# Performance work log

Measured on AMD Instinct MI355X. Metric: run time of the kernel, lower is better.

The kernel has to match this reference:

```python
import jax, jax.numpy as jnp
import numpy as np

N_EMBD = 1024
N_HEAD = 16
HEAD_DIM = N_EMBD // N_HEAD
NEG = -1e9


def setup_inputs() -> dict:
    key = jax.random.key(0)
    ks = jax.random.split(key, 5)
    B, S = 2, 2048
    x = jax.random.normal(ks[0], (B, S, N_EMBD), dtype=jnp.float32)
    # qkv_proj: Linear(n_embd, 3*n_embd) -> weight used as x @ W_qkv (W stored [in, out])
    scale = 1.0 / np.sqrt(N_EMBD)
    W_qkv = jax.random.normal(ks[1], (N_EMBD, 3 * N_EMBD), dtype=jnp.float32) * scale
    b_qkv = jax.random.normal(ks[2], (3 * N_EMBD,), dtype=jnp.float32) * 0.02
    W_out = jax.random.normal(ks[3], (N_EMBD, N_EMBD), dtype=jnp.float32) * scale
    b_out = jax.random.normal(ks[4], (N_EMBD,), dtype=jnp.float32) * 0.02
    return {"x": x, "W_qkv": W_qkv, "b_qkv": b_qkv, "W_out": W_out, "b_out": b_out}


def reference(x, W_qkv, b_qkv, W_out, b_out):
    B, S, E = x.shape
    qkv = x @ W_qkv + b_qkv                      # [B,S,3E]
    q, k, v = jnp.split(qkv, 3, axis=-1)
    # [B,S,E] -> [B,H,S,D]
    def split_heads(t):
        return t.reshape(B, S, N_HEAD, HEAD_DIM).transpose(0, 2, 1, 3)
    q, k, v = split_heads(q), split_heads(k), split_heads(v)
    scores = jnp.einsum("bhqd,bhkd->bhqk", q, k) / jnp.sqrt(jnp.float32(HEAD_DIM))
    causal = jnp.tril(jnp.ones((S, S), dtype=bool))
    scores = jnp.where(causal, scores, NEG)
    attn = jax.nn.softmax(scores, axis=-1)
    out = jnp.einsum("bhqk,bhkd->bhqd", attn, v)  # [B,H,S,D]
    out = out.transpose(0, 2, 1, 3).reshape(B, S, E)
    return out @ W_out + b_out
```

## Files before the change

kernel.cpp:

```cpp
#include <hip/hip_runtime.h>
#include <hip/hip_bf16.h>

#define BATCH 2
#define SEQ   2048
#define EMBD  1024
#define NHEAD 16
#define HDIM  64
#define QKV3  (3 * EMBD)

typedef __attribute__((ext_vector_type(8))) __bf16 bf16x8;
typedef __attribute__((ext_vector_type(4))) __bf16 bf16x4;
typedef __attribute__((ext_vector_type(4))) float f32x4;

#define QSCALE 0.18033688011112043f

__global__ __launch_bounds__(256) void cast_f32_bf16(
    const float* __restrict__ in, __bf16* __restrict__ out)
{
    int i = (blockIdx.x * 256 + threadIdx.x) * 8;
    float4 a = *(const float4*)&in[i];
    float4 b = *(const float4*)&in[i + 4];
    bf16x8 o;
    o[0] = (__bf16)a.x; o[1] = (__bf16)a.y; o[2] = (__bf16)a.z; o[3] = (__bf16)a.w;
    o[4] = (__bf16)b.x; o[5] = (__bf16)b.y; o[6] = (__bf16)b.z; o[7] = (__bf16)b.w;
    *(bf16x8*)&out[i] = o;
}

__global__ __launch_bounds__(256) void transpose_cast_bf16(
    const float* __restrict__ in, __bf16* __restrict__ out, int K, int N)
{
    __shared__ float t[64][65];
    const int k0 = blockIdx.y * 64, n0 = blockIdx.x * 64;
    const int tid = threadIdx.x;
    #pragma unroll
    for (int p = 0; p < 4; p++) {
        int kr = p * 16 + (tid >> 4);
        int c4 = (tid & 15) * 4;
        float4 v = *(const float4*)&in[(size_t)(k0 + kr) * N + n0 + c4];
        t[kr][c4] = v.x; t[kr][c4 + 1] = v.y; t[kr][c4 + 2] = v.z; t[kr][c4 + 3] = v.w;
    }
    __syncthreads();
    #pragma unroll
    for (int p = 0; p < 4; p++) {
        int nr = p * 16 + (tid >> 4);
        int k4 = (tid & 15) * 4;
        bf16x4 o;
        o[0] = (__bf16)t[k4 + 0][nr];
        o[1] = (__bf16)t[k4 + 1][nr];
        o[2] = (__bf16)t[k4 + 2][nr];
        o[3] = (__bf16)t[k4 + 3][nr];
        *(bf16x4*)&out[(size_t)(n0 + nr) * K + k0 + k4] = o;
    }
}

__global__ __launch_bounds__(256) void transpose_v_bf16(
    const __bf16* __restrict__ qkv, __bf16* __restrict__ vt)
{
    __shared__ __bf16 t[64][72];
    const int k0 = blockIdx.x * 64;
    const int bh = blockIdx.y;
    const int b = bh >> 4, h = bh & 15;
    const size_t base = (size_t)b * SEQ * QKV3 + 2 * EMBD + h * HDIM;
    const int tid = threadIdx.x;
    #pragma unroll
    for (int it = 0; it < 2; it++) {
        int flat = it * 256 + tid;
        int kr = flat >> 3;
        int d0 = (flat & 7) * 8;
        bf16x8 v = *(const bf16x8*)&qkv[base + (size_t)(k0 + kr) * QKV3 + d0];
        #pragma unroll
        for (int i = 0; i < 8; i++) t[kr][d0 + i] = v[i];
    }
    __syncthreads();
    #pragma unroll
    for (int it = 0; it < 2; it++) {
        int flat = it * 256 + tid;
        int d  = flat >> 3;
        int kc = (flat & 7) * 8;
        bf16x8 o;
        #pragma unroll
        for (int i = 0; i < 8; i++) o[i] = t[kc + i][d];
        *(bf16x8*)&vt[((size_t)bh * 64 + d) * SEQ + k0 + kc] = o;
    }
}

template<bool OUT_BF16>
__global__ __launch_bounds__(256) void gemm_bt_mfma(
    const __bf16* __restrict__ A,
    const __bf16* __restrict__ Bt,
    const float* __restrict__ bias,
    void* __restrict__ Cv,
    int M, int N, int K, int nscale)
{
    __shared__ __align__(16) __bf16 As[128 * 32];
    __shared__ __align__(16) __bf16 Bs[128 * 32];

    const int tid  = threadIdx.x;
    const int lane = tid & 63;
    const int wave = tid >> 6;
    const int wm = (wave >> 1) * 64;
    const int wn = (wave & 1) * 64;
    const int m0 = blockIdx.y * 128;
    const int n0 = blockIdx.x * 128;
    const int lm = lane & 15;
    const int kq = lane >> 4;

    f32x4 acc[4][4] = {};

    for (int k0 = 0; k0 < K; k0 += 32) {
        __syncthreads();
        #pragma unroll
        for (int r = 0; r < 2; r++) {
            int flat = r * 256 + tid;
            int row  = flat >> 2;
            int off  = (flat & 3) * 16;
            const char* ga = (const char*)(A + (size_t)(m0 + row) * K + k0) + off;
            char* la = (char*)As + flat * 16;
            __builtin_amdgcn_global_load_lds(
                (const __attribute__((address_space(1))) void*)ga,
                (__attribute__((address_space(3))) void*)la, 16, 0, 0);
            const char* gb = (const char*)(Bt + (size_t)(n0 + row) * K + k0) + off;
            char* lb = (char*)Bs + flat * 16;
            __builtin_amdgcn_global_load_lds(
                (const __attribute__((address_space(1))) void*)gb,
                (__attribute__((address_space(3))) void*)lb, 16, 0, 0);
        }
        __syncthreads();

        bf16x8 af[4], bf[4];
        #pragma unroll
        for (int t = 0; t < 4; t++) {
            af[t] = *(const bf16x8*)&As[(wm + t * 16 + lm) * 32 + kq * 8];
            bf[t] = *(const bf16x8*)&Bs[(wn + t * 16 + lm) * 32 + kq * 8];
        }
        #pragma unroll
        for (int i = 0; i < 4; i++)
            #pragma unroll
            for (int j = 0; j < 4; j++)
                acc[i][j] = __builtin_amdgcn_mfma_f32_16x16x32_bf16(
                    af[i], bf[j], acc[i][j], 0, 0, 0);
    }

    const int r0 = kq * 4;
    #pragma unroll
    for (int i = 0; i < 4; i++) {
        #pragma unroll
        for (int j = 0; j < 4; j++) {
            int col = n0 + wn + j * 16 + lm;
            float bv = bias[col];
            float sc = (col < nscale) ? QSCALE : 1.0f;
            #pragma unroll
            for (int r = 0; r < 4; r++) {
                int row = m0 + wm + i * 16 + r0 + r;
                float val = (acc[i][j][r] + bv) * sc;
                if (OUT_BF16) ((__bf16*)Cv)[(size_t)row * N + col] = (__bf16)val;
                else          ((float*)Cv)[(size_t)row * N + col] = val;
            }
        }
    }
}

__global__ __launch_bounds__(256, 3) void attn_kpar_mfma(
    const __bf16* __restrict__ qkv, const __bf16* __restrict__ vt,
    __bf16* __restrict__ attn)
{
    __shared__ __align__(16) char smem[16896];

    const int tid  = threadIdx.x;
    const int wave = tid >> 6;
    const int lane = tid & 63;
    const int quad = lane >> 4;
    const int c    = lane & 15;

    const int bh = blockIdx.x;
    const int b  = bh >> 4;
    const int h  = bh & 15;
    const int qblk = (int)(gridDim.y - 1) - blockIdx.y;
    const int q0 = qblk * 32;

    const size_t base = (size_t)b * SEQ * QKV3;
    const int hoff = h * HDIM;
    const __bf16* vbase = vt + (size_t)bh * 64 * SEQ;

    bf16x8 aq[2][2];
    #pragma unroll
    for (int qf = 0; qf < 2; qf++) {
        const __bf16* qrow = qkv + base +
            (size_t)(q0 + qf * 16 + c) * QKV3 + hoff + quad * 8;
        aq[qf][0] = *(const bf16x8*)(qrow);
        aq[qf][1] = *(const bf16x8*)(qrow + 32);
    }

    f32x4 acc[2][4] = {};
    float lpart[2][4] = {};

    char* pbw = smem + wave * 4096;
    const int ntiles = q0 / 64 + 1;

    for (int t = wave; t < ntiles; t += 4) {
        const int k0 = t * 64;
        const bool diag = (t == ntiles - 1);

        bf16x8 bk[4][2];
        #pragma unroll
        for (int jj = 0; jj < 4; jj++) {
            const __bf16* krow = qkv + base +
                (size_t)(k0 + jj * 16 + c) * QKV3 + EMBD + hoff + quad * 8;
            bk[jj][0] = *(const bf16x8*)(krow);
            bk[jj][1] = *(const bf16x8*)(krow + 32);
        }
        bf16x8 bv[4][2];
        #pragma unroll
        for (int dd = 0; dd < 4; dd++) {
            const __bf16* vr = vbase + (size_t)(dd * 16 + c) * SEQ + k0 + quad * 8;
            bv[dd][0] = *(const bf16x8*)(vr);
            bv[dd][1] = *(const bf16x8*)(vr + 32);
        }

        #pragma unroll
        for (int jj = 0; jj < 4; jj++) {
            const int col = jj * 16 + c;
            const int kabs_c = k0 + col;
            const int ab = (col >> 5) * 1024 + ((col >> 3) & 3) * 256 + (col & 7) * 2;
            #pragma unroll
            for (int qf = 0; qf < 2; qf++) {
                f32x4 s = {};
                s = __builtin_amdgcn_mfma_f32_16x16x32_bf16(aq[qf][0], bk[jj][0], s, 0, 0, 0);
                s = __builtin_amdgcn_mfma_f32_16x16x32_bf16(aq[qf][1], bk[jj][1], s, 0, 0, 0);
                char* pq = pbw + qf * 2048 + ab;
                const int qabs0 = q0 + qf * 16 + quad * 4;
                #pragma unroll
                for (int r = 0; r < 4; r++) {
                    float p;
                    if (diag && (kabs_c > qabs0 + r)) p = 0.f;
                    else p = __builtin_amdgcn_exp2f(s[r]);
                    lpart[qf][r] += p;
                    *(__bf16*)(pq + (quad * 4 + r) * 16) = (__bf16)p;
                }
            }
        }

        bf16x8 ap[2][2];
        #pragma unroll
        for (int qf = 0; qf < 2; qf++) {
            ap[qf][0] = *(const bf16x8*)(pbw + qf * 2048 + lane * 16);
            ap[qf][1] = *(const bf16x8*)(pbw + qf * 2048 + 1024 + lane * 16);
        }

        #pragma unroll
        for (int dd = 0; dd < 4; dd++) {
            #pragma unroll
            for (int qf = 0; qf < 2; qf++) {
                acc[qf][dd] = __builtin_amdgcn_mfma_f32_16x16x32_bf16(ap[qf][0], bv[dd][0], acc[qf][dd], 0, 0, 0);
                acc[qf][dd] = __builtin_amdgcn_mfma_f32_16x16x32_bf16(ap[qf][1], bv[dd][1], acc[qf][dd], 0, 0, 0);
            }
        }
    }

    #pragma unroll
    for (int qf = 0; qf < 2; qf++)
        #pragma unroll
        for (int r = 0; r < 4; r++) {
            float v = lpart[qf][r];
            v += __shfl_xor(v, 1);
            v += __shfl_xor(v, 2);
            v += __shfl_xor(v, 4);
            v += __shfl_xor(v, 8);
            lpart[qf][r] = v;
        }

    __syncthreads();

    float* Ored = (float*)smem;
    float* lred = (float*)(smem + 16640);

    if (wave < 2) {
        float* R = Ored + wave * (32 * 65);
        #pragma unroll
        for (int qf = 0; qf < 2; qf++)
            #pragma unroll
            for (int dd = 0; dd < 4; dd++)
                #pragma unroll
                for (int r = 0; r < 4; r++)
                    R[(qf * 16 + quad * 4 + r) * 65 + dd * 16 + c] = acc[qf][dd][r];
        if (c == 0) {
            #pragma unroll
            for (int qf = 0; qf < 2; qf++)
                #pragma unroll
                for (int r = 0; r < 4; r++)
                    lred[wave * 32 + qf * 16 + quad * 4 + r] = lpart[qf][r];
        }
    }
    __syncthreads();
    if (wave >= 2) {
        float* R = Ored + (wave - 2) * (32 * 65);
        #pragma unroll
        for (int qf = 0; qf < 2; qf++)
            #pragma unroll
            for (int dd = 0; dd < 4; dd++)
                #pragma unroll
                for (int r = 0; r < 4; r++)
                    R[(qf * 16 + quad * 4 + r) * 65 + dd * 16 + c] += acc[qf][dd][r];
        if (c == 0) {
            #pragma unroll
            for (int qf = 0; qf < 2; qf++)
                #pragma unroll
                for (int r = 0; r < 4; r++)
                    lred[(wave - 2) * 32 + qf * 16 + quad * 4 + r] += lpart[qf][r];
        }
    }
    __syncthreads();

    {
        const int row = tid >> 3;
        const int cg  = tid & 7;
        const float l = lred[row] + lred[32 + row];
        const float inv = 1.f / l;
        const float* R0 = Ored + row * 65 + cg * 8;
        const float* R1 = R0 + 32 * 65;
        bf16x8 o;
        #pragma unroll
        for (int i = 0; i < 8; i++) o[i] = (__bf16)((R0[i] + R1[i]) * inv);
        *(bf16x8*)&attn[((size_t)b * SEQ + q0 + row) * EMBD + hoff + cg * 8] = o;
    }
}

extern "C" void kernel_launch(void* const* d_in, const int* in_sizes, int n_in,
                              void* d_out, int out_size, void* d_ws, size_t ws_size,
                              hipStream_t stream)
{
    const float* x     = (const float*)d_in[0];
    const float* W_qkv = (const float*)d_in[1];
    const float* b_qkv = (const float*)d_in[2];
    const float* W_out = (const float*)d_in[3];
    const float* b_out = (const float*)d_in[4];
    float* out = (float*)d_out;

    const int M = BATCH * SEQ;

    __bf16* xbf    = (__bf16*)d_ws;
    __bf16* Wqkv_t = xbf    + (size_t)M * EMBD;
    __bf16* Wout_t = Wqkv_t + (size_t)QKV3 * EMBD;
    __bf16* qkv    = Wout_t + (size_t)EMBD * EMBD;
    __bf16* attn   = qkv    + (size_t)M * QKV3;
    __bf16* vtbuf  = attn   + (size_t)M * EMBD;

    cast_f32_bf16<<<(M * EMBD) / (256 * 8), 256, 0, stream>>>(x, xbf);
    {
        dim3 g(QKV3 / 64, EMBD / 64);
        transpose_cast_bf16<<<g, 256, 0, stream>>>(W_qkv, Wqkv_t, EMBD, QKV3);
    }
    {
        dim3 g(EMBD / 64, EMBD / 64);
        transpose_cast_bf16<<<g, 256, 0, stream>>>(W_out, Wout_t, EMBD, EMBD);
    }
    {
        dim3 grid(QKV3 / 128, M / 128);
        gemm_bt_mfma<true><<<grid, 256, 0, stream>>>(xbf, Wqkv_t, b_qkv, qkv, M, QKV3, EMBD, EMBD);
    }
    {
        dim3 grid(SEQ / 64, BATCH * NHEAD);
        transpose_v_bf16<<<grid, 256, 0, stream>>>(qkv, vtbuf);
    }
    {
        dim3 grid(BATCH * NHEAD, SEQ / 32);
        attn_kpar_mfma<<<grid, 256, 0, stream>>>(qkv, vtbuf, attn);
    }
    {
        dim3 grid(EMBD / 128, M / 128);
        gemm_bt_mfma<false><<<grid, 256, 0, stream>>>(attn, Wout_t, b_out, out, M, EMBD, EMBD, 0);
    }
}
```

Before: 226.3 us.

## Fuse V transpose and head-major Q/K layout into QKV GEMM epilogue

The QKV projection GEMM now writes Q and K directly in head-major [B,H,S,D] layout and writes V already transposed into the [B,H,D,S] buffer. This removes the separate V-transpose kernel launch and its extra read/write of V. The attention kernel reads contiguous per-head Q/K rows instead of strided rows of the packed qkv buffer. The V epilogue stores are 4-element vectors strided by SEQ per lane, and the Q/K stores are scalar and scattered, so the GEMM's write pattern may become less coalesced.

After: 220.1 us. 2.7% less time.

```diff
diff --git a/kernel.cpp b/kernel.cpp
--- a/kernel.cpp
+++ b/kernel.cpp
@@ -53,45 +53,13 @@
     }
 }
 
-__global__ __launch_bounds__(256) void transpose_v_bf16(
-    const __bf16* __restrict__ qkv, __bf16* __restrict__ vt)
-{
-    __shared__ __bf16 t[64][72];
-    const int k0 = blockIdx.x * 64;
-    const int bh = blockIdx.y;
-    const int b = bh >> 4, h = bh & 15;
-    const size_t base = (size_t)b * SEQ * QKV3 + 2 * EMBD + h * HDIM;
-    const int tid = threadIdx.x;
-    #pragma unroll
-    for (int it = 0; it < 2; it++) {
-        int flat = it * 256 + tid;
-        int kr = flat >> 3;
-        int d0 = (flat & 7) * 8;
-        bf16x8 v = *(const bf16x8*)&qkv[base + (size_t)(k0 + kr) * QKV3 + d0];
-        #pragma unroll
-        for (int i = 0; i < 8; i++) t[kr][d0 + i] = v[i];
-    }
-    __syncthreads();
-    #pragma unroll
-    for (int it = 0; it < 2; it++) {
-        int flat = it * 256 + tid;
-        int d  = flat >> 3;
-        int kc = (flat & 7) * 8;
-        bf16x8 o;
-        #pragma unroll
-        for (int i = 0; i < 8; i++) o[i] = t[kc + i][d];
-        *(bf16x8*)&vt[((size_t)bh * 64 + d) * SEQ + k0 + kc] = o;
-    }
-}
-
-template<bool OUT_BF16>
-__global__ __launch_bounds__(256) void gemm_bt_mfma(
+__global__ __launch_bounds__(256) void gemm_qkv_mfma(
     const __bf16* __restrict__ A,
     const __bf16* __restrict__ Bt,
     const float* __restrict__ bias,
-    void* __restrict__ Cv,
-    int M, int N, int K, int nscale)
-{
+    __bf16* __restrict__ qh, __bf16* __restrict__ kh, __bf16* __restrict__ vt)
+{
+    const int N = QKV3, K = EMBD;
     __shared__ __align__(16) __bf16 As[128 * 32];
     __shared__ __align__(16) __bf16 Bs[128 * 32];
 
@@ -144,25 +112,108 @@
     const int r0 = kq * 4;
     #pragma unroll
     for (int i = 0; i < 4; i++) {
+        const int row0 = m0 + wm + i * 16 + r0;
+        const int b  = row0 >> 11;
+        const int s0 = row0 & 2047;
+        #pragma unroll
+        for (int j = 0; j < 4; j++) {
+            const int col = n0 + wn + j * 16 + lm;
+            const float bv = bias[col];
+            const int region = col >> 10;
+            const int hh = (col >> 6) & 15;
+            const int dd = col & 63;
+            const size_t bh = (size_t)(b * 16 + hh);
+            if (region == 2) {
+                bf16x4 o;
+                #pragma unroll
+                for (int r = 0; r < 4; r++) o[r] = (__bf16)(acc[i][j][r] + bv);
+                *(bf16x4*)&vt[(bh * 64 + dd) * SEQ + s0] = o;
+            } else {
+                __bf16* dst = (region == 0) ? qh : kh;
+                const float sc = (region == 0) ? QSCALE : 1.0f;
+                #pragma unroll
+                for (int r = 0; r < 4; r++)
+                    dst[(bh * SEQ + s0 + r) * 64 + dd] = (__bf16)((acc[i][j][r] + bv) * sc);
+            }
+        }
+    }
+}
+
+__global__ __launch_bounds__(256) void gemm_bt_mfma_f32out(
+    const __bf16* __restrict__ A,
+    const __bf16* __restrict__ Bt,
+    const float* __restrict__ bias,
+    float* __restrict__ C,
+    int M, int N, int K)
+{
+    __shared__ __align__(16) __bf16 As[128 * 32];
+    __shared__ __align__(16) __bf16 Bs[128 * 32];
+
+    const int tid  = threadIdx.x;
+    const int lane = tid & 63;
+    const int wave = tid >> 6;
+    const int wm = (wave >> 1) * 64;
+    const int wn = (wave & 1) * 64;
+    const int m0 = blockIdx.y * 128;
+    const int n0 = blockIdx.x * 128;
+    const int lm = lane & 15;
+    const int kq = lane >> 4;
+
+    f32x4 acc[4][4] = {};
+
+    for (int k0 = 0; k0 < K; k0 += 32) {
+        __syncthreads();
+        #pragma unroll
+        for (int r = 0; r < 2; r++) {
+            int flat = r * 256 + tid;
+            int row  = flat >> 2;
+            int off  = (flat & 3) * 16;
+            const char* ga = (const char*)(A + (size_t)(m0 + row) * K + k0) + off;
+            char* la = (char*)As + flat * 16;
+            __builtin_amdgcn_global_load_lds(
+                (const __attribute__((address_space(1))) void*)ga,
+                (__attribute__((address_space(3))) void*)la, 16, 0, 0);
+            const char* gb = (const char*)(Bt + (size_t)(n0 + row) * K + k0) + off;
+            char* lb = (char*)Bs + flat * 16;
+            __builtin_amdgcn_global_load_lds(
+                (const __attribute__((address_space(1))) void*)gb,
+                (__attribute__((address_space(3))) void*)lb, 16, 0, 0);
+        }
+        __syncthreads();
+
+        bf16x8 af[4], bf[4];
+        #pragma unroll
+        for (int t = 0; t < 4; t++) {
+            af[t] = *(const bf16x8*)&As[(wm + t * 16 + lm) * 32 + kq * 8];
+            bf[t] = *(const bf16x8*)&Bs[(wn + t * 16 + lm) * 32 + kq * 8];
+        }
+        #pragma unroll
+        for (int i = 0; i < 4; i++)
+            #pragma unroll
+            for (int j = 0; j < 4; j++)
+                acc[i][j] = __builtin_amdgcn_mfma_f32_16x16x32_bf16(
+                    af[i], bf[j], acc[i][j], 0, 0, 0);
+    }
+
+    const int r0 = kq * 4;
+    #pragma unroll
+    for (int i = 0; i < 4; i++) {
         #pragma unroll
         for (int j = 0; j < 4; j++) {
             int col = n0 + wn + j * 16 + lm;
             float bv = bias[col];
-            float sc = (col < nscale) ? QSCALE : 1.0f;
             #pragma unroll
             for (int r = 0; r < 4; r++) {
                 int row = m0 + wm + i * 16 + r0 + r;
-                float val = (acc[i][j][r] + bv) * sc;
-                if (OUT_BF16) ((__bf16*)Cv)[(size_t)row * N + col] = (__bf16)val;
-                else          ((float*)Cv)[(size_t)row * N + col] = val;
+                C[(size_t)row * N + col] = acc[i][j][r] + bv;
             }
         }
     }
 }
 
 __global__ __launch_bounds__(256, 3) void attn_kpar_mfma(
-    const __bf16* __restrict__ qkv, const __bf16* __restrict__ vt,
-    __bf16* __restrict__ attn)
+    const __bf16* __restrict__ qh, const __bf16* __restrict__ kh,
+    const __bf16* __restrict__ vt, __bf16* __restrict__ attn)
 {
     __shared__ __align__(16) char smem[16896];
 
@@ -178,15 +229,15 @@
     const int qblk = (int)(gridDim.y - 1) - blockIdx.y;
     const int q0 = qblk * 32;
 
-    const size_t base = (size_t)b * SEQ * QKV3;
     const int hoff = h * HDIM;
+    const __bf16* qbase = qh + (size_t)bh * SEQ * 64;
+    const __bf16* kbase = kh + (size_t)bh * SEQ * 64;
     const __bf16* vbase = vt + (size_t)bh * 64 * SEQ;
 
     bf16x8 aq[2][2];
     #pragma unroll
     for (int qf = 0; qf < 2; qf++) {
-        const __bf16* qrow = qkv + base +
-            (size_t)(q0 + qf * 16 + c) * QKV3 + hoff + quad * 8;
+        const __bf16* qrow = qbase + (size_t)(q0 + qf * 16 + c) * 64 + quad * 8;
         aq[qf][0] = *(const bf16x8*)(qrow);
         aq[qf][1] = *(const bf16x8*)(qrow + 32);
     }
@@ -204,8 +255,7 @@
         bf16x8 bk[4][2];
         #pragma unroll
         for (int jj = 0; jj < 4; jj++) {
-            const __bf16* krow = qkv + base +
-                (size_t)(k0 + jj * 16 + c) * QKV3 + EMBD + hoff + quad * 8;
+            const __bf16* krow = kbase + (size_t)(k0 + jj * 16 + c) * 64 + quad * 8;
             bk[jj][0] = *(const bf16x8*)(krow);
             bk[jj][1] = *(const bf16x8*)(krow + 32);
         }
@@ -341,9 +391,10 @@
     __bf16* xbf    = (__bf16*)d_ws;
     __bf16* Wqkv_t = xbf    + (size_t)M * EMBD;
     __bf16* Wout_t = Wqkv_t + (size_t)QKV3 * EMBD;
-    __bf16* qkv    = Wout_t + (size_t)EMBD * EMBD;
-    __bf16* attn   = qkv    + (size_t)M * QKV3;
-    __bf16* vtbuf  = attn   + (size_t)M * EMBD;
+    __bf16* qh     = Wout_t + (size_t)EMBD * EMBD;
+    __bf16* kh     = qh     + (size_t)M * EMBD;
+    __bf16* vtbuf  = kh     + (size_t)M * EMBD;
+    __bf16* attn   = vtbuf  + (size_t)M * EMBD;
 
     cast_f32_bf16<<<(M * EMBD) / (256 * 8), 256, 0, stream>>>(x, xbf);
     {
@@ -356,18 +407,14 @@
     }
     {
         dim3 grid(QKV3 / 128, M / 128);
-        gemm_bt_mfma<true><<<grid, 256, 0, stream>>>(xbf, Wqkv_t, b_qkv, qkv, M, QKV3, EMBD, EMBD);
-    }
-    {
-        dim3 grid(SEQ / 64, BATCH * NHEAD);
-        transpose_v_bf16<<<grid, 256, 0, stream>>>(qkv, vtbuf);
+        gemm_qkv_mfma<<<grid, 256, 0, stream>>>(xbf, Wqkv_t, b_qkv, qh, kh, vtbuf);
     }
     {
         dim3 grid(BATCH * NHEAD, SEQ / 32);
-        attn_kpar_mfma<<<grid, 256, 0, stream>>>(qkv, vtbuf, attn);
+        attn_kpar_mfma<<<grid, 256, 0, stream>>>(qh, kh, vtbuf, attn);
     }
     {
         dim3 grid(EMBD / 128, M / 128);
-        gemm_bt_mfma<false><<<grid, 256, 0, stream>>>(attn, Wout_t, b_out, out, M, EMBD, EMBD, 0);
-    }
-}
+        gemm_bt_mfma_f32out<<<grid, 256, 0, stream>>>(attn, Wout_t, b_out, out, M, EMBD, EMBD);
+    }
+}
```
